# Kernel tuning notes

Hardware: AMD Instinct MI355X
Metric: run time of the kernel (lower is better)

## Reference

```python
import jax, jax.numpy as jnp
import numpy as np

BS, D, N, E, L, NE = 8, 512, 2048, 8, 64, 524288


def conv1d_same(x, w, b):
    # x: [B, W, Cin], w: [K, Cin, Cout] -> [B, W, Cout], stride 1, 'same' padding
    y = jax.lax.conv_general_dilated(x, w, window_strides=(1,), padding='SAME',
                                     dimension_numbers=('NWC', 'WIO', 'NWC'))
    return y + b


def setup_inputs() -> dict:
    key = jax.random.key(0)
    ks = jax.random.split(key, 10)
    def nrm(k, shape, s=1.0):
        return jax.random.normal(k, shape, jnp.float32) * s
    return {
        'latent': nrm(ks[0], (BS, D)),
        'edge_index': jax.random.randint(ks[1], (2, NE), 0, BS * N),
        'W_dense': nrm(ks[2], (D, N), 0.05),
        'b_dense': jnp.zeros((N,), jnp.float32),
        'conv1_w': nrm(ks[3], (3, 1, E), 0.3),
        'conv1_b': jnp.zeros((E,), jnp.float32),
        'gat_Wq': nrm(ks[4], (E, E), 0.3),
        'gat_bq': jnp.zeros((E,), jnp.float32),
        'gat_Wk': nrm(ks[5], (E, E), 0.3),
        'gat_bk': jnp.zeros((E,), jnp.float32),
        'gat_Wv': nrm(ks[6], (E, E), 0.3),
        'gat_bias': jnp.zeros((E,), jnp.float32),
        'qkv_w': nrm(ks[7], (3, E, 3 * E * L), 0.1),
        'qkv_b': jnp.zeros((3 * E * L,), jnp.float32),
    }


def reference(latent, edge_index, W_dense, b_dense, conv1_w, conv1_b,
              gat_Wq, gat_bq, gat_Wk, gat_bk, gat_Wv, gat_bias, qkv_w, qkv_b):
    bs = latent.shape[0]
    # Dense -> [bs, N], expand -> Conv1D(E) -> [bs, N, E]
    skeleton = latent @ W_dense + b_dense
    skeleton = conv1d_same(skeleton[..., None], conv1_w, conv1_b)
    # concat(unstack, axis=0) == reshape to batched graph nodes [bs*N, E]
    x = skeleton.reshape(bs * N, E)
    BN = bs * N
    # GAT (tf_geometric, num_heads=1): add self-loops, per-edge dot-attention,
    # segment softmax over destination (row), scatter-sum aggregate.
    loops = jnp.arange(BN)
    row = jnp.concatenate([edge_index[0], loops])
    col = jnp.concatenate([edge_index[1], loops])
    Q = jax.nn.leaky_relu(x @ gat_Wq + gat_bq, 0.2)
    K = jax.nn.leaky_relu(x @ gat_Wk + gat_bk, 0.2)
    V = x @ gat_Wv
    score = jnp.sum(Q[row] * K[col], axis=-1)            # [n_edges + BN]
    smax = jax.ops.segment_max(score, row, num_segments=BN)
    ex = jnp.exp(score - smax[row])
    ssum = jax.ops.segment_sum(ex, row, num_segments=BN)
    alpha = ex / ssum[row]                               # segment softmax
    h = jax.ops.segment_sum(alpha[:, None] * V[col], row, num_segments=BN) + gat_bias
    graph = h.reshape(bs, N, E)                          # stack(split(., bs))
    # QVK conv over node axis -> [bs, N, 3*E*L]
    qvk = conv1d_same(graph, qkv_w, qkv_b)
    # stack(split(., L, -1), 1) then concat(unstack(., -2), -1)
    qvk = qvk.reshape(bs, N, L, 3 * E).transpose(0, 2, 1, 3).reshape(bs, L, N * 3 * E)
    q, v, k = jnp.split(qvk, 3, axis=-1)                 # each [bs, L, N*E]
    # keras Attention (use_scale=False): softmax(q @ k^T) @ v
    attn = jax.nn.softmax(jnp.einsum('btd,bsd->bts', q, k), axis=-1)
    seq = jnp.einsum('bts,bsd->btd', attn, v)
    # stack(split(., N, -1), -2) == reshape [bs, L, N, E]
    return seq.reshape(bs, L, N, E)
```

## Files before the change

### kernel.cpp

```cpp
#include <hip/hip_runtime.h>
#include <hip/hip_bf16.h>
#include <math.h>

#define BSZ 8
#define DDIM 512
#define NND 2048
#define EE 8
#define LLH 64
#define NEDGE 524288
#define BNN 16384
#define OCC 1536
#define DQ 16384

typedef __attribute__((ext_vector_type(8))) short short8;

__device__ inline unsigned short f2bf(float x) {
    __hip_bfloat16 h = __float2bfloat16(x);
    return __builtin_bit_cast(unsigned short, h);
}
__device__ inline float bf2f(unsigned short u) {
    return __uint_as_float(((unsigned int)u) << 16);
}

__global__ __launch_bounds__(256) void k_densep(const float* __restrict__ latent,
                                                const float* __restrict__ Wd,
                                                float* __restrict__ pdense,
                                                int* __restrict__ hist) {
    int n0 = blockIdx.x * 32, d0 = blockIdx.y * 64;
    __shared__ float lat[8][64];
    int tid = threadIdx.x;
    if (blockIdx.y == 0) hist[blockIdx.x * 256 + tid] = 0;
    #pragma unroll
    for (int r = 0; r < 2; ++r) {
        int i = r * 256 + tid;
        lat[i >> 6][i & 63] = latent[(i >> 6) * DDIM + d0 + (i & 63)];
    }
    __syncthreads();
    int nl = tid & 31, b = tid >> 5;
    const float* wp = Wd + (size_t)d0 * NND + n0 + nl;
    float acc = 0.f;
    #pragma unroll 8
    for (int d = 0; d < 64; ++d) acc += lat[b][d] * wp[(size_t)d * NND];
    pdense[((size_t)blockIdx.y * BSZ + b) * NND + n0 + nl] = acc;
}

__global__ __launch_bounds__(64) void k_gat(const float* __restrict__ pdense,
                                            const float* __restrict__ bd,
                                            const float* __restrict__ w1,
                                            const float* __restrict__ b1,
                                            const float* __restrict__ Wq, const float* __restrict__ bq,
                                            const float* __restrict__ Wk, const float* __restrict__ bk,
                                            const float* __restrict__ Wv,
                                            const int* __restrict__ ei,
                                            float* __restrict__ Qg, float* __restrict__ Kg,
                                            float* __restrict__ Vg, int* __restrict__ hist) {
    int i = blockIdx.x * 64 + threadIdx.x;
    int b = i >> 11, n = i & (NND - 1);
    float sm = 0.f, s0 = 0.f, sp = 0.f;
    #pragma unroll
    for (int ds = 0; ds < 8; ++ds) {
        const float* p = pdense + ((size_t)ds * BSZ + b) * NND + n;
        if (n > 0) sm += p[-1];
        s0 += p[0];
        if (n < NND - 1) sp += p[1];
    }
    if (n > 0) sm += bd[n - 1];
    s0 += bd[n];
    if (n < NND - 1) sp += bd[n + 1];
    float xr[EE];
    #pragma unroll
    for (int e = 0; e < EE; ++e)
        xr[e] = sm * w1[e] + s0 * w1[EE + e] + sp * w1[2 * EE + e] + b1[e];
    #pragma unroll
    for (int j = 0; j < EE; ++j) {
        float q = bq[j], k = bk[j], v = 0.f;
        #pragma unroll
        for (int c = 0; c < EE; ++c) {
            q += xr[c] * Wq[c * EE + j];
            k += xr[c] * Wk[c * EE + j];
            v += xr[c] * Wv[c * EE + j];
        }
        Qg[(size_t)i * EE + j] = (q >= 0.f) ? q : 0.2f * q;
        Kg[(size_t)i * EE + j] = (k >= 0.f) ? k : 0.2f * k;
        Vg[(size_t)i * EE + j] = v;
    }
    #pragma unroll 4
    for (int j = 0; j < 32; ++j)
        atomicAdd(hist + ei[i + j * BNN], 1);
}

__global__ __launch_bounds__(1024) void k_scan(const int* __restrict__ hist,
                                               int* __restrict__ offs,
                                               int* __restrict__ cnt) {
    int tid = threadIdx.x;
    int lane = tid & 63, wv = tid >> 6;
    const int4* hp = (const int4*)(hist + tid * 16);
    int4 a = hp[0], b4 = hp[1], c4 = hp[2], d4 = hp[3];
    int h[16] = {a.x, a.y, a.z, a.w, b4.x, b4.y, b4.z, b4.w,
                 c4.x, c4.y, c4.z, c4.w, d4.x, d4.y, d4.z, d4.w};
    int mysum = 0;
    #pragma unroll
    for (int i = 0; i < 16; ++i) mysum += h[i];
    int inc = mysum;
    #pragma unroll
    for (int off = 1; off < 64; off <<= 1) {
        int u = __shfl_up(inc, off, 64);
        if (lane >= off) inc += u;
    }
    __shared__ int wtot[16];
    if (lane == 63) wtot[wv] = inc;
    __syncthreads();
    if (tid < 16) {
        int t = wtot[tid];
        #pragma unroll
        for (int off = 1; off < 16; off <<= 1) {
            int u = __shfl_up(t, off, 16);
            if (tid >= off) t += u;
        }
        wtot[tid] = t;
    }
    __syncthreads();
    int run = (wv ? wtot[wv - 1] : 0) + inc - mysum;
    #pragma unroll
    for (int i = 0; i < 16; ++i) {
        offs[tid * 16 + i] = run;
        cnt[tid * 16 + i] = run;
        run += h[i];
    }
}

__global__ void k_scatter(const int* __restrict__ ei, int* __restrict__ cnt,
                          int* __restrict__ ecol) {
    int e = blockIdx.x * 256 + threadIdx.x;
    if (e >= NEDGE) return;
    int r = ei[e], c = ei[NEDGE + e];
    int pos = atomicAdd(cnt + r, 1);
    ecol[pos] = c;
}

__global__ __launch_bounds__(256) void k_gatagg(const int* __restrict__ ecol,
                                                const int* __restrict__ offs,
                                                const int* __restrict__ hist,
                                                const float* __restrict__ Qg,
                                                const float* __restrict__ Kg,
                                                const float* __restrict__ Vg,
                                                const float* __restrict__ gbias,
                                                float* __restrict__ hg) {
    int row = __builtin_amdgcn_readfirstlane(blockIdx.x * 4 + (threadIdx.x >> 6));
    int lane = threadIdx.x & 63;
    const float* Qr = Qg + (size_t)row * EE;
    float q0 = Qr[0], q1 = Qr[1], q2 = Qr[2], q3 = Qr[3];
    float q4 = Qr[4], q5 = Qr[5], q6 = Qr[6], q7 = Qr[7];
    int beg = offs[row], deg = hist[row];
    int total = deg + 1;
    float m = -INFINITY, l = 0.f;
    float acc[EE];
    #pragma unroll
    for (int j = 0; j < EE; ++j) acc[j] = 0.f;
    for (int base = 0; base < total; base += 64) {
        int idx = base + lane;
        int c = row;
        if (idx < deg) c = ecol[beg + idx];
        const float4* K4 = (const float4*)(Kg + (size_t)c * EE);
        float4 ka = K4[0], kb = K4[1];
        float s = q0*ka.x + q1*ka.y + q2*ka.z + q3*ka.w
                + q4*kb.x + q5*kb.y + q6*kb.z + q7*kb.w;
        if (idx >= total) s = -INFINITY;
        float pm = s;
        #pragma unroll
        for (int off = 32; off > 0; off >>= 1) pm = fmaxf(pm, __shfl_xor(pm, off));
        float nm = fmaxf(m, pm);
        float scale = __expf(m - nm);
        float p = (idx < total) ? __expf(s - nm) : 0.f;
        float ps = p;
        #pragma unroll
        for (int off = 32; off > 0; off >>= 1) ps += __shfl_xor(ps, off);
        l = l * scale + ps;
        const float4* V4 = (const float4*)(Vg + (size_t)c * EE);
        float4 va = V4[0], vb = V4[1];
        float pv[EE] = {p*va.x, p*va.y, p*va.z, p*va.w, p*vb.x, p*vb.y, p*vb.z, p*vb.w};
        #pragma unroll
        for (int j = 0; j < EE; ++j) {
            float t = pv[j];
            #pragma unroll
            for (int off = 32; off > 0; off >>= 1) t += __shfl_xor(t, off);
            acc[j] = acc[j] * scale + t;
        }
        m = nm;
    }
    if (lane < EE)
        hg[(size_t)row * EE + lane] = acc[lane] / l + gbias[lane];
}

__global__ __launch_bounds__(256) void k_qkvFvM(const float* __restrict__ hg,
                                                const float* __restrict__ qw,
                                                const float* __restrict__ qb,
                                                unsigned short* __restrict__ Fq,
                                                float* __restrict__ Mpart) {
    int bx = blockIdx.x, b = blockIdx.y, tid = threadIdx.x;
    if (bx < 22) {
        int n0 = 682 + bx * 32;
        __shared__ float hs[34 * EE];
        __shared__ unsigned short st[32 * 768];
        for (int i = tid; i < 34 * EE; i += 256) {
            int nn = n0 - 1 + (i >> 3);
            hs[i] = (nn >= 0 && nn < NND) ? hg[((size_t)b * NND + nn) * EE + (i & 7)] : 0.f;
        }
        __syncthreads();
        #pragma unroll
        for (int pass = 0; pass < 2; ++pass) {
            if (pass) __syncthreads();
            float w[3][24], bias[3];
            #pragma unroll
            for (int rr = 0; rr < 3; ++rr) {
                int o = pass * 768 + rr * 256 + tid;
                bias[rr] = qb[o];
                #pragma unroll
                for (int kk = 0; kk < 24; ++kk) w[rr][kk] = qw[kk * OCC + o];
            }
            for (int nn = 0; nn < 32; ++nn) {
                const float* hv = &hs[nn * EE];
                float a0 = bias[0], a1 = bias[1], a2 = bias[2];
                #pragma unroll
                for (int kk = 0; kk < 24; ++kk) {
                    float h = hv[kk];
                    a0 += h * w[0][kk]; a1 += h * w[1][kk]; a2 += h * w[2][kk];
                }
                st[nn * 768 + tid]       = f2bf(a0);
                st[nn * 768 + tid + 256] = f2bf(a1);
                st[nn * 768 + tid + 512] = f2bf(a2);
            }
            __syncthreads();
            unsigned short* dstbase = Fq + ((size_t)b * NND + n0) * OCC + pass * 768;
            #pragma unroll
            for (int it = 0; it < 12; ++it) {
                int idx8 = it * 256 + tid;
                int row = idx8 / 96, col8 = idx8 - row * 96;
                if (n0 + row <= 1365)
                    *(short8*)(dstbase + (size_t)row * OCC + col8 * 8) =
                        *(const short8*)(&st[row * 768 + col8 * 8]);
            }
        }
    } else {
        int sp = bx - 22;
        int nq0 = sp * 86;
        __shared__ float hq[88][EE];
        __shared__ float hk[90][EE];
        for (int i = tid; i < 88 * EE; i += 256) {
            int r = nq0 - 1 + (i >> 3);
            hq[i >> 3][i & 7] = (r >= 0 && r < NND) ? hg[((size_t)b * NND + r) * EE + (i & 7)] : 0.f;
        }
        for (int i = tid; i < 90 * EE; i += 256) {
            int r = nq0 + 1364 + (i >> 3);
            hk[i >> 3][i & 7] = (r < NND) ? hg[((size_t)b * NND + r) * EE + (i & 7)] : 0.f;
        }
        __syncthreads();
        int cnt1 = 683 - nq0; if (cnt1 > 86) cnt1 = 86; if (cnt1 < 0) cnt1 = 0;
        int cnt2 = 682 - nq0; if (cnt2 > 86) cnt2 = 86; if (cnt2 < 0) cnt2 = 0;
        for (int idx = tid; idx < 1250; idx += 256) {
            int mm = idx / 625, p = idx - (idx / 625) * 625;
            int i = p / 25, j = p - (p / 25) * 25;
            int cnt = mm ? cnt2 : cnt1;
            int qi = i >> 3, qe = i & 7;
            int kj = (j >> 3) + mm, ke = j & 7;
            float acc = 0.f;
            if (i < 24 && j < 24) {
                for (int nl = 0; nl < cnt; ++nl)
                    acc += hq[nl + qi][qe] * hk[nl + kj][ke];
            } else if (i < 24) {
                for (int nl = 0; nl < cnt; ++nl) acc += hq[nl + qi][qe];
            } else if (j < 24) {
                for (int nl = 0; nl < cnt; ++nl) acc += hk[nl + kj][ke];
            } else {
                acc = (float)cnt;
            }
            Mpart[((size_t)(sp * 8 + b)) * 1250 + idx] = acc;
        }
    }
}

__global__ __launch_bounds__(256) void k_Ssm(const float* __restrict__ qw,
                                             const float* __restrict__ qb,
                                             const float* __restrict__ Mpart,
                                             float* __restrict__ atT) {
    __shared__ float Ms[8][1250];
    __shared__ float As[25 * 24];
    __shared__ float T1[8][25 * 24];
    int t = blockIdx.x, tid = threadIdx.x;
    for (int idx = tid; idx < 10000; idx += 256) {
        int b = idx / 1250, r = idx - (idx / 1250) * 1250;
        float s = 0.f;
        #pragma unroll
        for (int sp = 0; sp < 8; ++sp)
            s += Mpart[((size_t)(sp * 8 + b)) * 1250 + r];
        Ms[b][r] = s;
    }
    for (int idx = tid; idx < 600; idx += 256) {
        int i = idx / 24, c = idx - (idx / 24) * 24;
        As[idx] = (i < 24) ? qw[i * OCC + t * 24 + c] : qb[t * 24 + c];
    }
    __syncthreads();
    for (int idx = tid; idx < 4800; idx += 256) {
        int b = idx / 600, rem = idx - (idx / 600) * 600;
        int j = rem / 24, c = rem - (rem / 24) * 24;
        int mo = (c < 16) ? 0 : 625;
        float acc = 0.f;
        #pragma unroll 5
        for (int i = 0; i < 25; ++i)
            acc += Ms[b][mo + i * 25 + j] * As[i * 24 + c];
        T1[b][j * 24 + c] = acc;
    }
    __syncthreads();
    int s = tid & 63, bg = tid >> 6;
    float acc0 = 0.f, acc1 = 0.f;
    for (int j = 0; j < 25; ++j) {
        float Bv[24];
        const float* bp = (j < 24) ? (qw + (size_t)j * OCC + s * 24) : (qb + s * 24);
        #pragma unroll
        for (int r = 0; r < 6; ++r) {
            float4 v = *(const float4*)(bp + r * 4);
            Bv[r*4+0]=v.x; Bv[r*4+1]=v.y; Bv[r*4+2]=v.z; Bv[r*4+3]=v.w;
        }
        const float* t1a = &T1[bg][j * 24];
        const float* t1b = &T1[bg + 4][j * 24];
        #pragma unroll
        for (int c = 0; c < 16; ++c) {
            acc0 += t1a[c] * Bv[8 + c];
            acc1 += t1b[c] * Bv[8 + c];
        }
        #pragma unroll
        for (int c = 16; c < 24; ++c) {
            acc0 += t1a[c] * Bv[c - 16];
            acc1 += t1b[c] * Bv[c - 16];
        }
    }
    #pragma unroll
    for (int r = 0; r < 2; ++r) {
        int b = bg + r * 4;
        float v = r ? acc1 : acc0;
        float m = v;
        #pragma unroll
        for (int off = 32; off > 0; off >>= 1) m = fmaxf(m, __shfl_xor(m, off));
        float e = __expf(v - m);
        float sum = e;
        #pragma unroll
        for (int off = 32; off > 0; off >>= 1) sum += __shfl_xor(sum, off);
        atT[((size_t)b * LLH + s) * LLH + t] = e / sum;
    }
}

__global__ __launch_bounds__(256) void k_attnV(const unsigned short* __restrict__ Fq,
                                               const float* __restrict__ atT,
                                               float* __restrict__ out) {
    int b = blockIdx.y;
    int d0 = blockIdx.x * 64;
    int tid = threadIdx.x;
    __shared__ unsigned short vt[64 * 64];
    const unsigned short* Fb = Fq + (size_t)b * NND * OCC;
    #pragma unroll
    for (int r = 0; r < 16; ++r) {
        int idx = r * 256 + tid;
        int s = idx >> 6, d = idx & 63;
        int f = DQ + d0 + d;
        int n = f / 24, c = f - n * 24;
        vt[s * 64 + d] = Fb[(size_t)n * OCC + s * 24 + c];
    }
    __syncthreads();
    int lane = tid & 63;
    int t0 = __builtin_amdgcn_readfirstlane((tid >> 6) * 16);
    const float* arow = atT + (size_t)b * LLH * LLH + t0;
    float acc[16];
    #pragma unroll
    for (int tt = 0; tt < 16; ++tt) acc[tt] = 0.f;
    #pragma unroll 4
    for (int s = 0; s < LLH; ++s) {
        float vv = bf2f(vt[s * 64 + lane]);
        #pragma unroll
        for (int tt = 0; tt < 16; ++tt)
            acc[tt] += arow[s * LLH + tt] * vv;
    }
    float* ob = out + ((size_t)b * LLH + t0) * DQ + d0 + lane;
    #pragma unroll
    for (int tt = 0; tt < 16; ++tt) ob[(size_t)tt * DQ] = acc[tt];
}

extern "C" void kernel_launch(void* const* d_in, const int* in_sizes, int n_in,
                              void* d_out, int out_size, void* d_ws, size_t ws_size,
                              hipStream_t stream) {
    (void)in_sizes; (void)n_in; (void)out_size; (void)ws_size;
    const float* latent = (const float*)d_in[0];
    const int*   ei     = (const int*)d_in[1];
    const float* Wd     = (const float*)d_in[2];
    const float* bd     = (const float*)d_in[3];
    const float* w1     = (const float*)d_in[4];
    const float* b1     = (const float*)d_in[5];
    const float* Wq     = (const float*)d_in[6];
    const float* bq     = (const float*)d_in[7];
    const float* Wk     = (const float*)d_in[8];
    const float* bk     = (const float*)d_in[9];
    const float* Wv     = (const float*)d_in[10];
    const float* gbias  = (const float*)d_in[11];
    const float* qw     = (const float*)d_in[12];
    const float* qb     = (const float*)d_in[13];
    float* out = (float*)d_out;

    float* ws     = (float*)d_ws;
    float* pdense = ws;
    float* Qg     = pdense + 64 * NND;
    float* Kg     = Qg + BNN * EE;
    float* Vg     = Kg + BNN * EE;
    float* hg     = Vg + BNN * EE;
    int*   hist   = (int*)(hg + BNN * EE);
    int*   offs   = hist + BNN;
    int*   cnt    = offs + BNN;
    int*   ecol   = cnt + BNN;
    float* Mp     = (float*)(ecol + NEDGE);
    float* atT    = Mp + 80000;
    unsigned short* Fq = (unsigned short*)(atT + BSZ * LLH * LLH);

    k_densep<<<dim3(64, 8), dim3(256), 0, stream>>>(latent, Wd, pdense, hist);
    k_gat<<<dim3(256), dim3(64), 0, stream>>>(pdense, bd, w1, b1, Wq, bq, Wk, bk, Wv,
                                              ei, Qg, Kg, Vg, hist);
    k_scan<<<dim3(1), dim3(1024), 0, stream>>>(hist, offs, cnt);
    k_scatter<<<dim3(NEDGE / 256), dim3(256), 0, stream>>>(ei, cnt, ecol);
    k_gatagg<<<dim3(BNN / 4), dim3(256), 0, stream>>>(ecol, offs, hist,
                                                      Qg, Kg, Vg, gbias, hg);
    k_qkvFvM<<<dim3(30, 8), dim3(256), 0, stream>>>(hg, qw, qb, Fq, Mp);
    k_Ssm<<<dim3(64), dim3(256), 0, stream>>>(qw, qb, Mp, atT);
    k_attnV<<<dim3(256, 8), dim3(256), 0, stream>>>(Fq, atT, out);
}
```

Baseline: 148.2 us.

## Fuse QKV/M-partial and score-softmax kernels via grid barrier; store V transposed

Merges the conv/M-partial kernel and the score+softmax kernel into one launch. The 64 M-partial blocks sync through an atomic grid barrier and then compute the attention weights, while the other blocks write the V features. V is now stored transposed ([b][d][s] bf16), so the attnV kernel can load it with vector reads instead of a strided gather. This removes one launch and the uncoalesced V gather. The barrier assumes all 64 barrier blocks are co-resident and adds spin-wait overhead.

```diff
diff --git a/kernel.cpp b/kernel.cpp
--- a/kernel.cpp
+++ b/kernel.cpp
@@ -13,6 +13,7 @@
 #define DQ 16384
 
 typedef __attribute__((ext_vector_type(8))) short short8;
+typedef __attribute__((ext_vector_type(4))) unsigned short ushort4v;
 
 __device__ inline unsigned short f2bf(float x) {
     __hip_bfloat16 h = __float2bfloat16(x);
@@ -22,14 +23,27 @@
     return __uint_as_float(((unsigned int)u) << 16);
 }
 
+__device__ inline void gridbar64(int* c) {
+    __syncthreads();
+    if (threadIdx.x == 0) {
+        __threadfence();
+        atomicAdd(c, 1);
+        while (atomicAdd(c, 0) < 64) __builtin_amdgcn_s_sleep(8);
+        __threadfence();
+    }
+    __syncthreads();
+}
+
 __global__ __launch_bounds__(256) void k_densep(const float* __restrict__ latent,
                                                 const float* __restrict__ Wd,
                                                 float* __restrict__ pdense,
-                                                int* __restrict__ hist) {
+                                                int* __restrict__ hist,
+                                                int* __restrict__ cbar) {
     int n0 = blockIdx.x * 32, d0 = blockIdx.y * 64;
     __shared__ float lat[8][64];
     int tid = threadIdx.x;
     if (blockIdx.y == 0) hist[blockIdx.x * 256 + tid] = 0;
+    if (blockIdx.x == 0 && blockIdx.y == 0 && tid < 16) cbar[tid] = 0;
     #pragma unroll
     for (int r = 0; r < 2; ++r) {
         int i = r * 256 + tid;
@@ -192,21 +206,27 @@
         hg[(size_t)row * EE + lane] = acc[lane] / l + gbias[lane];
 }
 
-__global__ __launch_bounds__(256) void k_qkvFvM(const float* __restrict__ hg,
-                                                const float* __restrict__ qw,
-                                                const float* __restrict__ qb,
-                                                unsigned short* __restrict__ Fq,
-                                                float* __restrict__ Mpart) {
-    int bx = blockIdx.x, b = blockIdx.y, tid = threadIdx.x;
-    if (bx < 22) {
-        int n0 = 682 + bx * 32;
-        __shared__ float hs[34 * EE];
-        __shared__ unsigned short st[32 * 768];
+__global__ __launch_bounds__(256) void k_midfuse(const float* __restrict__ hg,
+                                                 const float* __restrict__ qw,
+                                                 const float* __restrict__ qb,
+                                                 unsigned short* __restrict__ FvT,
+                                                 float* __restrict__ Mpart,
+                                                 float* __restrict__ atT,
+                                                 int* __restrict__ cbar) {
+    __shared__ float smem[16064];
+    int bid = blockIdx.x, tid = threadIdx.x;
+    if (bid >= 64) {
+        int u = bid - 64;
+        int cx = u % 22, b = u / 22;
+        int n0 = 682 + cx * 32;
+        float* hs = smem;
+        unsigned short* st = (unsigned short*)(smem + 272);
         for (int i = tid; i < 34 * EE; i += 256) {
             int nn = n0 - 1 + (i >> 3);
             hs[i] = (nn >= 0 && nn < NND) ? hg[((size_t)b * NND + nn) * EE + (i & 7)] : 0.f;
         }
         __syncthreads();
+        int dbase = n0 * 24 - DQ;
         #pragma unroll
         for (int pass = 0; pass < 2; ++pass) {
             if (pass) __syncthreads();
@@ -231,28 +251,32 @@
                 st[nn * 768 + tid + 512] = f2bf(a2);
             }
             __syncthreads();
-            unsigned short* dstbase = Fq + ((size_t)b * NND + n0) * OCC + pass * 768;
-            #pragma unroll
-            for (int it = 0; it < 12; ++it) {
-                int idx8 = it * 256 + tid;
-                int row = idx8 / 96, col8 = idx8 - row * 96;
-                if (n0 + row <= 1365)
-                    *(short8*)(dstbase + (size_t)row * OCC + col8 * 8) =
-                        *(const short8*)(&st[row * 768 + col8 * 8]);
+            int l0 = pass * 32;
+            #pragma unroll
+            for (int it = 0; it < 24; ++it) {
+                int idx4 = it * 256 + tid;
+                int dl = idx4 >> 3, s4 = idx4 & 7;
+                int d = dbase + dl;
+                if (d < 0 || d >= DQ) continue;
+                int nn = dl / 24, c = dl - nn * 24;
+                const unsigned short* sb = st + nn * 768 + c;
+                ushort4v v4 = { sb[(s4 * 4 + 0) * 24], sb[(s4 * 4 + 1) * 24],
+                                sb[(s4 * 4 + 2) * 24], sb[(s4 * 4 + 3) * 24] };
+                *(ushort4v*)(FvT + ((size_t)b * DQ + d) * 64 + l0 + s4 * 4) = v4;
             }
         }
     } else {
-        int sp = bx - 22;
+        int sp = bid >> 3, b = bid & 7;
         int nq0 = sp * 86;
-        __shared__ float hq[88][EE];
-        __shared__ float hk[90][EE];
+        float* hq = smem;
+        float* hk = smem + 704;
         for (int i = tid; i < 88 * EE; i += 256) {
             int r = nq0 - 1 + (i >> 3);
-            hq[i >> 3][i & 7] = (r >= 0 && r < NND) ? hg[((size_t)b * NND + r) * EE + (i & 7)] : 0.f;
+            hq[i] = (r >= 0 && r < NND) ? hg[((size_t)b * NND + r) * EE + (i & 7)] : 0.f;
         }
         for (int i = tid; i < 90 * EE; i += 256) {
             int r = nq0 + 1364 + (i >> 3);
-            hk[i >> 3][i & 7] = (r < NND) ? hg[((size_t)b * NND + r) * EE + (i & 7)] : 0.f;
+            hk[i] = (r < NND) ? hg[((size_t)b * NND + r) * EE + (i & 7)] : 0.f;
         }
         __syncthreads();
         int cnt1 = 683 - nq0; if (cnt1 > 86) cnt1 = 86; if (cnt1 < 0) cnt1 = 0;
@@ -266,104 +290,99 @@
             float acc = 0.f;
             if (i < 24 && j < 24) {
                 for (int nl = 0; nl < cnt; ++nl)
-                    acc += hq[nl + qi][qe] * hk[nl + kj][ke];
+                    acc += hq[(nl + qi) * EE + qe] * hk[(nl + kj) * EE + ke];
             } else if (i < 24) {
-                for (int nl = 0; nl < cnt; ++nl) acc += hq[nl + qi][qe];
+                for (int nl = 0; nl < cnt; ++nl) acc += hq[(nl + qi) * EE + qe];
             } else if (j < 24) {
-                for (int nl = 0; nl < cnt; ++nl) acc += hk[nl + kj][ke];
+                for (int nl = 0; nl < cnt; ++nl) acc += hk[(nl + kj) * EE + ke];
             } else {
                 acc = (float)cnt;
             }
             Mpart[((size_t)(sp * 8 + b)) * 1250 + idx] = acc;
         }
-    }
-}
-
-__global__ __launch_bounds__(256) void k_Ssm(const float* __restrict__ qw,
-                                             const float* __restrict__ qb,
-                                             const float* __restrict__ Mpart,
-                                             float* __restrict__ atT) {
-    __shared__ float Ms[8][1250];
-    __shared__ float As[25 * 24];
-    __shared__ float T1[8][25 * 24];
-    int t = blockIdx.x, tid = threadIdx.x;
-    for (int idx = tid; idx < 10000; idx += 256) {
-        int b = idx / 1250, r = idx - (idx / 1250) * 1250;
-        float s = 0.f;
-        #pragma unroll
-        for (int sp = 0; sp < 8; ++sp)
-            s += Mpart[((size_t)(sp * 8 + b)) * 1250 + r];
-        Ms[b][r] = s;
-    }
-    for (int idx = tid; idx < 600; idx += 256) {
-        int i = idx / 24, c = idx - (idx / 24) * 24;
-        As[idx] = (i < 24) ? qw[i * OCC + t * 24 + c] : qb[t * 24 + c];
-    }
-    __syncthreads();
-    for (int idx = tid; idx < 4800; idx += 256) {
-        int b = idx / 600, rem = idx - (idx / 600) * 600;
-        int j = rem / 24, c = rem - (rem / 24) * 24;
-        int mo = (c < 16) ? 0 : 625;
-        float acc = 0.f;
-        #pragma unroll 5
-        for (int i = 0; i < 25; ++i)
-            acc += Ms[b][mo + i * 25 + j] * As[i * 24 + c];
-        T1[b][j * 24 + c] = acc;
-    }
-    __syncthreads();
-    int s = tid & 63, bg = tid >> 6;
-    float acc0 = 0.f, acc1 = 0.f;
-    for (int j = 0; j < 25; ++j) {
-        float Bv[24];
-        const float* bp = (j < 24) ? (qw + (size_t)j * OCC + s * 24) : (qb + s * 24);
-        #pragma unroll
-        for (int r = 0; r < 6; ++r) {
-            float4 v = *(const float4*)(bp + r * 4);
-            Bv[r*4+0]=v.x; Bv[r*4+1]=v.y; Bv[r*4+2]=v.z; Bv[r*4+3]=v.w;
-        }
-        const float* t1a = &T1[bg][j * 24];
-        const float* t1b = &T1[bg + 4][j * 24];
-        #pragma unroll
-        for (int c = 0; c < 16; ++c) {
-            acc0 += t1a[c] * Bv[8 + c];
-            acc1 += t1b[c] * Bv[8 + c];
-        }
-        #pragma unroll
-        for (int c = 16; c < 24; ++c) {
-            acc0 += t1a[c] * Bv[c - 16];
-            acc1 += t1b[c] * Bv[c - 16];
-        }
-    }
-    #pragma unroll
-    for (int r = 0; r < 2; ++r) {
-        int b = bg + r * 4;
-        float v = r ? acc1 : acc0;
-        float m = v;
-        #pragma unroll
-        for (int off = 32; off > 0; off >>= 1) m = fmaxf(m, __shfl_xor(m, off));
-        float e = __expf(v - m);
-        float sum = e;
-        #pragma unroll
-        for (int off = 32; off > 0; off >>= 1) sum += __shfl_xor(sum, off);
-        atT[((size_t)b * LLH + s) * LLH + t] = e / sum;
-    }
-}
-
-__global__ __launch_bounds__(256) void k_attnV(const unsigned short* __restrict__ Fq,
+        gridbar64(cbar);
+        int t = bid;
+        float* Ms = smem;
+        float* As = smem + 10000;
+        float* T1 = smem + 10600;
+        for (int idx = tid; idx < 10000; idx += 256) {
+            int b2 = idx / 1250, r = idx - (idx / 1250) * 1250;
+            float s = 0.f;
+            #pragma unroll
+            for (int sp2 = 0; sp2 < 8; ++sp2)
+                s += Mpart[((size_t)(sp2 * 8 + b2)) * 1250 + r];
+            Ms[b2 * 1250 + r] = s;
+        }
+        for (int idx = tid; idx < 600; idx += 256) {
+            int i = idx / 24, c = idx - (idx / 24) * 24;
+            As[idx] = (i < 24) ? qw[i * OCC + t * 24 + c] : qb[t * 24 + c];
+        }
+        __syncthreads();
+        for (int idx = tid; idx < 4800; idx += 256) {
+            int b2 = idx / 600, rem = idx - (idx / 600) * 600;
+            int j = rem / 24, c = rem - (rem / 24) * 24;
+            int mo = (c < 16) ? 0 : 625;
+            float acc = 0.f;
+            #pragma unroll 5
+            for (int i = 0; i < 25; ++i)
+                acc += Ms[b2 * 1250 + mo + i * 25 + j] * As[i * 24 + c];
+            T1[b2 * 600 + j * 24 + c] = acc;
+        }
+        __syncthreads();
+        int s = tid & 63, bg = tid >> 6;
+        float acc0 = 0.f, acc1 = 0.f;
+        for (int j = 0; j < 25; ++j) {
+            float Bv[24];
+            const float* bp = (j < 24) ? (qw + (size_t)j * OCC + s * 24) : (qb + s * 24);
+            #pragma unroll
+            for (int r = 0; r < 6; ++r) {
+                float4 v = *(const float4*)(bp + r * 4);
+                Bv[r*4+0]=v.x; Bv[r*4+1]=v.y; Bv[r*4+2]=v.z; Bv[r*4+3]=v.w;
+            }
+            const float* t1a = &T1[bg * 600 + j * 24];
+            const float* t1b = &T1[(bg + 4) * 600 + j * 24];
+            #pragma unroll
+            for (int c = 0; c < 16; ++c) {
+                acc0 += t1a[c] * Bv[8 + c];
+                acc1 += t1b[c] * Bv[8 + c];
+            }
+            #pragma unroll
+            for (int c = 16; c < 24; ++c) {
+                acc0 += t1a[c] * Bv[c - 16];
+                acc1 += t1b[c] * Bv[c - 16];
+            }
+        }
+        #pragma unroll
+        for (int r = 0; r < 2; ++r) {
+            int b2 = bg + r * 4;
+            float v = r ? acc1 : acc0;
+            float m = v;
+            #pragma unroll
+            for (int off = 32; off > 0; off >>= 1) m = fmaxf(m, __shfl_xor(m, off));
+            float e = __expf(v - m);
+            float sum = e;
+            #pragma unroll
+            for (int off = 32; off > 0; off >>= 1) sum += __shfl_xor(sum, off);
+            atT[((size_t)b2 * LLH + s) * LLH + t] = e / sum;
+        }
+    }
+}
+
+__global__ __launch_bounds__(256) void k_attnV(const unsigned short* __restrict__ FvT,
                                                const float* __restrict__ atT,
                                                float* __restrict__ out) {
     int b = blockIdx.y;
     int d0 = blockIdx.x * 64;
     int tid = threadIdx.x;
-    __shared__ unsigned short vt[64 * 64];
-    const unsigned short* Fb = Fq + (size_t)b * NND * OCC;
-    #pragma unroll
-    for (int r = 0; r < 16; ++r) {
+    __shared__ float vtf[64][65];
+    #pragma unroll
+    for (int r = 0; r < 2; ++r) {
         int idx = r * 256 + tid;
-        int s = idx >> 6, d = idx & 63;
-        int f = DQ + d0 + d;
-        int n = f / 24, c = f - n * 24;
-        vt[s * 64 + d] = Fb[(size_t)n * OCC + s * 24 + c];
+        int dl = idx >> 3, g = idx & 7;
+        short8 v = *(const short8*)(FvT + ((size_t)b * DQ + d0 + dl) * 64 + g * 8);
+        #pragma unroll
+        for (int j = 0; j < 8; ++j)
+            vtf[dl][g * 8 + j] = bf2f((unsigned short)v[j]);
     }
     __syncthreads();
     int lane = tid & 63;
@@ -374,7 +393,7 @@
     for (int tt = 0; tt < 16; ++tt) acc[tt] = 0.f;
     #pragma unroll 4
     for (int s = 0; s < LLH; ++s) {
-        float vv = bf2f(vt[s * 64 + lane]);
+        float vv = vtf[lane][s];
         #pragma unroll
         for (int tt = 0; tt < 16; ++tt)
             acc[tt] += arow[s * LLH + tt] * vv;
@@ -414,18 +433,18 @@
     int*   offs   = hist + BNN;
     int*   cnt    = offs + BNN;
     int*   ecol   = cnt + BNN;
-    float* Mp     = (float*)(ecol + NEDGE);
+    int*   cbar   = ecol + NEDGE;
+    float* Mp     = (float*)(cbar + 16);
     float* atT    = Mp + 80000;
-    unsigned short* Fq = (unsigned short*)(atT + BSZ * LLH * LLH);
-
-    k_densep<<<dim3(64, 8), dim3(256), 0, stream>>>(latent, Wd, pdense, hist);
+    unsigned short* FvT = (unsigned short*)(atT + BSZ * LLH * LLH);
+
+    k_densep<<<dim3(64, 8), dim3(256), 0, stream>>>(latent, Wd, pdense, hist, cbar);
     k_gat<<<dim3(256), dim3(64), 0, stream>>>(pdense, bd, w1, b1, Wq, bq, Wk, bk, Wv,
                                               ei, Qg, Kg, Vg, hist);
     k_scan<<<dim3(1), dim3(1024), 0, stream>>>(hist, offs, cnt);
     k_scatter<<<dim3(NEDGE / 256), dim3(256), 0, stream>>>(ei, cnt, ecol);
     k_gatagg<<<dim3(BNN / 4), dim3(256), 0, stream>>>(ecol, offs, hist,
                                                       Qg, Kg, Vg, gbias, hg);
-    k_qkvFvM<<<dim3(30, 8), dim3(256), 0, stream>>>(hg, qw, qb, Fq, Mp);
-    k_Ssm<<<dim3(64), dim3(256), 0, stream>>>(qw, qb, Mp, atT);
-    k_attnV<<<dim3(256, 8), dim3(256), 0, stream>>>(Fq, atT, out);
-}
+    k_midfuse<<<dim3(240), dim3(256), 0, stream>>>(hg, qw, qb, FvT, Mp, atT, cbar);
+    k_attnV<<<dim3(256, 8), dim3(256), 0, stream>>>(FvT, atT, out);
+}
```

Result: no change. 147.3 us (-0.6%).
